# Kernel tuning notes

Measured on AMD Instinct MI355X. Metric: run time of the kernel, lower is better.

Reference implementation:

```python
import jax, jax.numpy as jnp
import numpy as np

N_COUNTS = 6  # pyramid levels (original + 5 sum-pools)


def _sum_pool2(x):
    # 2x2x2 sum pooling (AvgPool3d with divisor_override=1)
    B, C, D, H, W = x.shape
    return x.reshape(B, C, D // 2, 2, H // 2, 2, W // 2, 2).sum(axis=(3, 5, 7))


def _forward(image, bounds):
    n = N_COUNTS
    q = jnp.log(2.0 ** jnp.arange(n, dtype=jnp.float32))  # (S,)
    qs = q.sum()
    q2s = (q * q).sum()
    qs2 = qs * qs
    kf = bounds.astype(jnp.float32)  # (K,)
    # prefactor a: 1 for k==1 (entropy branch), else 1/(k-1); inf at k==1 masked by where
    a = jnp.where(bounds == 1, 1.0, 1.0 / jnp.where(bounds == 1, jnp.inf, kf - 1.0))

    # normalizer b = sum of nonzero entries of finest map == total sum
    b = image.sum(axis=(2, 3, 4))  # (B, C)

    maps = [image]
    for _ in range(n - 1):
        maps.append(_sum_pool2(maps[-1]))

    ps = []
    for m in maps:
        x = m.reshape(m.shape[0], m.shape[1], -1)  # (B, C, V)
        mask = x != 0
        xn = x / b[:, :, None]
        safe = jnp.where(mask, xn, 1.0)  # 1.0 placeholder at zeros, masked out below
        # generic branch (k != 1): p = log(sum over nonzero of (x/b)**k)
        pw = safe[:, :, :, None] ** kf  # (B, C, V, K)
        s = jnp.sum(jnp.where(mask[..., None], pw, 0.0), axis=2)  # (B, C, K)
        p_gen = jnp.log(s)
        # k == 1 branch: p = sum over nonzero of xn * log(xn)
        p_one = jnp.sum(jnp.where(mask, xn * jnp.log(safe), 0.0), axis=2)  # (B, C)
        ps.append(jnp.where(bounds == 1, p_one[:, :, None], p_gen))

    p_all = jnp.stack(ps, axis=-1)  # (B, C, K, S)
    # least-squares slope of p vs q; a00 = min(S, ql) = n
    num = n * jnp.einsum('bcks,s->bck', p_all, q) - p_all.sum(axis=-1) * qs
    den = n * q2s - qs2
    return a * num / den  # (B, C, K)


def setup_inputs() -> dict:
    key = jax.random.key(0)
    k1, _ = jax.random.split(key)
    image = jax.random.uniform(k1, (2, 3, 128, 128, 128), dtype=jnp.float32)
    bounds = jnp.arange(8, dtype=jnp.int32) - 2  # [-2..5]
    return {"image": image, "bounds": bounds}


def reference(image, bounds):
    return _forward(image, bounds)
```

## Files before the change

### kernel.cpp

```cpp
#include <hip/hip_runtime.h>

#define CHVOL (128*128*128)

__device__ __forceinline__ void accum9(float* a, float x) {
    bool nz = (x != 0.0f);
    float u = nz ? __builtin_amdgcn_rcpf(x) : 0.0f;
    float l = nz ? __logf(x) : 0.0f;
    float x2 = x * x;
    float x4 = x2 * x2;
    a[0] = fmaf(u, u, a[0]);
    a[1] += u;
    a[2] += nz ? 1.0f : 0.0f;
    a[3] += x;
    a[4] += x2;
    a[5] = fmaf(x2, x, a[5]);
    a[6] += x4;
    a[7] = fmaf(x4, x, a[7]);
    a[8] = fmaf(x, l, a[8]);
}

template<int NS>
__device__ __forceinline__ void wave_reduce(float* acc) {
    #pragma unroll
    for (int s = 0; s < NS; ++s) {
        float v = acc[s];
        v += __shfl_down(v, 32, 64);
        v += __shfl_down(v, 16, 64);
        v += __shfl_down(v, 8, 64);
        v += __shfl_down(v, 4, 64);
        v += __shfl_down(v, 2, 64);
        v += __shfl_down(v, 1, 64);
        acc[s] = v;
    }
}

template<int NS>
__device__ __forceinline__ void block_reduce(float* acc, float* red, int t) {
    #pragma unroll
    for (int s = 0; s < NS; ++s) {
        float v = acc[s];
        v += __shfl_down(v, 32, 64);
        v += __shfl_down(v, 16, 64);
        v += __shfl_down(v, 8, 64);
        v += __shfl_down(v, 4, 64);
        v += __shfl_down(v, 2, 64);
        v += __shfl_down(v, 1, 64);
        if ((t & 63) == 0) red[(t >> 6) * NS + s] = v;
    }
    __syncthreads();
}

__global__ __launch_bounds__(256) void k_main(const float* __restrict__ img,
                                              float* __restrict__ part,
                                              float* __restrict__ l3map) {
    __shared__ float zm[256];
    __shared__ float red[36 * 4];

    const int t  = threadIdx.x;
    const int l  = t & 63, w = t >> 6;
    const int r  = blockIdx.x;
    const int ch = blockIdx.y;
    const int ry = r & 15, rz = r >> 4;
    const float* base = img + (size_t)ch * CHVOL + rz * (8 * 16384) + ry * (8 * 128);

    float acc[36];
    #pragma unroll
    for (int j = 0; j < 36; ++j) acc[j] = 0.0f;

    const int x5 = l & 31;
    const int y  = ((l >> 5) & 1) | (w << 1);
    const float* tbase = base + y * 128 + x5 * 4;

    float4 v[8];
    #pragma unroll
    for (int i = 0; i < 8; ++i) v[i] = *(const float4*)(tbase + i * 16384);

    float d0 = 0.0f, d1 = 0.0f;
    float ca = 0.0f, cb = 0.0f;
    #pragma unroll
    for (int i = 0; i < 8; ++i) {
        accum9(acc, v[i].x); accum9(acc, v[i].y); accum9(acc, v[i].z); accum9(acc, v[i].w);
        float a = v[i].x + v[i].y, b = v[i].z + v[i].w;
        a += __shfl_xor(a, 32, 64);
        b += __shfl_xor(b, 32, 64);
        if ((i & 1) == 0) { ca = a; cb = b; }
        else {
            float A = ca + a, B = cb + b;
            accum9(acc + 9, A); accum9(acc + 9, B);
            if (i < 4) d0 += A + B; else d1 += A + B;
        }
    }
    #pragma unroll
    for (int j = 9; j < 18; ++j) acc[j] *= 0.5f;

    if ((l >> 5) == 0) {
        zm[w * 64 + x5]      = d0;
        zm[w * 64 + 32 + x5] = d1;
    }
    __syncthreads();

    if (t < 128) {
        int x = t & 31, zpp = (t >> 5) & 1, ypp = t >> 6;
        float s = zm[(2 * ypp) * 64 + zpp * 32 + x] + zm[(2 * ypp + 1) * 64 + zpp * 32 + x];
        accum9(acc + 18, s);
    }
    if (t < 16) {
        float s = 0.0f;
        #pragma unroll
        for (int q = 0; q < 8; ++q)
            s += zm[q * 32 + 2 * t] + zm[q * 32 + 2 * t + 1];
        accum9(acc + 27, s);
        l3map[(size_t)ch * 4096 + rz * 256 + ry * 16 + t] = s;
    }

    block_reduce<36>(acc, red, t);
    if (t < 36)
        part[((size_t)ch * 36 + t) * 256 + r] =
            red[t] + red[36 + t] + red[72 + t] + red[108 + t];
}

__global__ __launch_bounds__(512) void k_fin(const float* __restrict__ part,
                                             const float* __restrict__ l3map,
                                             const int* __restrict__ bounds,
                                             float* __restrict__ out) {
    __shared__ float M4[512];
    __shared__ float redA[36 * 4];
    __shared__ float redB[9 * 4];
    __shared__ float sst[54];

    const int t  = threadIdx.x;
    const int ch = blockIdx.x;

    if (t < 256) {
        float acc[36];
        #pragma unroll
        for (int j = 0; j < 36; ++j)
            acc[j] = part[((size_t)ch * 36 + j) * 256 + t];
        wave_reduce<36>(acc);
        if ((t & 63) == 0) {
            #pragma unroll
            for (int s = 0; s < 36; ++s) redA[(t >> 6) * 36 + s] = acc[s];
        }
    } else {
        const float2* L3 = (const float2*)(l3map + (size_t)ch * 4096);
        const int th = t - 256;
        float a9[9];
        #pragma unroll
        for (int j = 0; j < 9; ++j) a9[j] = 0.0f;
        #pragma unroll
        for (int i = 0; i < 2; ++i) {
            int c = th + i * 256;
            int x = c & 7, y = (c >> 3) & 7, z = c >> 6;
            const float2* p = L3 + z * 256 + y * 16 + x;
            float2 b0 = p[0], b1 = p[8], b2 = p[128], b3 = p[136];
            float s = (b0.x + b0.y) + (b1.x + b1.y) + (b2.x + b2.y) + (b3.x + b3.y);
            M4[c] = s;
            accum9(a9, s);
        }
        wave_reduce<9>(a9);
        if ((t & 63) == 0) {
            #pragma unroll
            for (int s = 0; s < 9; ++s) redB[((t >> 6) - 4) * 9 + s] = a9[s];
        }
    }
    __syncthreads();

    if (t < 36) sst[t] = redA[t] + redA[36 + t] + redA[72 + t] + redA[108 + t];
    if (t >= 36 && t < 45) {
        int s = t - 36;
        sst[36 + s] = redB[s] + redB[9 + s] + redB[18 + s] + redB[27 + s];
    }
    if (t < 64) {
        float c9[9];
        #pragma unroll
        for (int j = 0; j < 9; ++j) c9[j] = 0.0f;
        int x = t & 3, y = (t >> 2) & 3, z = t >> 4;
        const float2* p = (const float2*)M4 + z * 64 + y * 8 + x;
        float2 b0 = p[0], b1 = p[4], b2 = p[32], b3 = p[36];
        float s = (b0.x + b0.y) + (b1.x + b1.y) + (b2.x + b2.y) + (b3.x + b3.y);
        accum9(c9, s);
        wave_reduce<9>(c9);
        if (t == 0) {
            #pragma unroll
            for (int j = 0; j < 9; ++j) sst[45 + j] = c9[j];
        }
    }
    __syncthreads();

    if (t < 8) {
        int k = bounds[t];
        const double LN2 = 0.6931471805599453094;
        double b  = (double)sst[3];
        double lb = log(b);
        double num = 0.0;
        #pragma unroll
        for (int s = 0; s < 6; ++s) {
            const float* st = sst + s * 9;
            double p;
            if (k == 1) p = ((double)st[8] - lb * (double)st[3]) / b;
            else        p = log((double)st[k + 2]) - (double)k * lb;
            num += (6.0 * s - 15.0) * LN2 * p;
        }
        double den = 105.0 * LN2 * LN2;
        double aa  = (k == 1) ? 1.0 : 1.0 / (double)(k - 1);
        out[ch * 8 + t] = (float)(aa * num / den);
    }
}

extern "C" void kernel_launch(void* const* d_in, const int* in_sizes, int n_in,
                              void* d_out, int out_size, void* d_ws, size_t ws_size,
                              hipStream_t stream) {
    const float* img    = (const float*)d_in[0];
    const int*   bounds = (const int*)d_in[1];
    float*       out    = (float*)d_out;
    float*       ws     = (float*)d_ws;

    float* part  = ws;
    float* l3map = ws + 55296;

    k_main<<<dim3(256, 6), 256, 0, stream>>>(img, part, l3map);
    k_fin<<<6, 512, 0, stream>>>(part, l3map, bounds, out);
}
```

Baseline: 110.9 us.

## Remap threads so each owns a 2x2 y-z column, dropping level-1 shuffles

Each thread now loads 4 z-slices by 2 y-rows of a float4 column instead of 8 z-slices of one row. This lets it form complete 2x2x2 level-1 sums in registers, with no cross-lane shuffle exchange. The halving scale and the conditional even/odd pairing go away, and every thread writes one level-2 partial into shared memory. The trade-off is a less contiguous per-warp load pattern (two rows per z-slice rather than one), which could change coalescing.

```diff
diff --git a/kernel.cpp b/kernel.cpp
--- a/kernel.cpp
+++ b/kernel.cpp
@@ -57,46 +57,43 @@
     __shared__ float red[36 * 4];
 
     const int t  = threadIdx.x;
-    const int l  = t & 63, w = t >> 6;
     const int r  = blockIdx.x;
     const int ch = blockIdx.y;
     const int ry = r & 15, rz = r >> 4;
-    const float* base = img + (size_t)ch * CHVOL + rz * (8 * 16384) + ry * (8 * 128);
+
+    const int x5 = t & 31;
+    const int yp = (t >> 5) & 3;
+    const int zq = t >> 7;
+
+    const float* tb = img + (size_t)ch * CHVOL + rz * (8 * 16384) + ry * (8 * 128)
+                    + (zq * 4) * 16384 + (yp * 2) * 128 + x5 * 4;
 
     float acc[36];
     #pragma unroll
     for (int j = 0; j < 36; ++j) acc[j] = 0.0f;
 
-    const int x5 = l & 31;
-    const int y  = ((l >> 5) & 1) | (w << 1);
-    const float* tbase = base + y * 128 + x5 * 4;
-
     float4 v[8];
     #pragma unroll
-    for (int i = 0; i < 8; ++i) v[i] = *(const float4*)(tbase + i * 16384);
-
-    float d0 = 0.0f, d1 = 0.0f;
-    float ca = 0.0f, cb = 0.0f;
+    for (int dz = 0; dz < 4; ++dz)
+        #pragma unroll
+        for (int dy = 0; dy < 2; ++dy)
+            v[dz * 2 + dy] = *(const float4*)(tb + dz * 16384 + dy * 128);
+
     #pragma unroll
     for (int i = 0; i < 8; ++i) {
         accum9(acc, v[i].x); accum9(acc, v[i].y); accum9(acc, v[i].z); accum9(acc, v[i].w);
-        float a = v[i].x + v[i].y, b = v[i].z + v[i].w;
-        a += __shfl_xor(a, 32, 64);
-        b += __shfl_xor(b, 32, 64);
-        if ((i & 1) == 0) { ca = a; cb = b; }
-        else {
-            float A = ca + a, B = cb + b;
-            accum9(acc + 9, A); accum9(acc + 9, B);
-            if (i < 4) d0 += A + B; else d1 += A + B;
-        }
-    }
-    #pragma unroll
-    for (int j = 9; j < 18; ++j) acc[j] *= 0.5f;
-
-    if ((l >> 5) == 0) {
-        zm[w * 64 + x5]      = d0;
-        zm[w * 64 + 32 + x5] = d1;
-    }
+    }
+
+    float ax[8], bx[8];
+    #pragma unroll
+    for (int i = 0; i < 8; ++i) { ax[i] = v[i].x + v[i].y; bx[i] = v[i].z + v[i].w; }
+    float A0 = (ax[0] + ax[1]) + (ax[2] + ax[3]);
+    float B0 = (bx[0] + bx[1]) + (bx[2] + bx[3]);
+    float A1 = (ax[4] + ax[5]) + (ax[6] + ax[7]);
+    float B1 = (bx[4] + bx[5]) + (bx[6] + bx[7]);
+    accum9(acc + 9, A0); accum9(acc + 9, B0); accum9(acc + 9, A1); accum9(acc + 9, B1);
+
+    zm[yp * 64 + zq * 32 + x5] = (A0 + B0) + (A1 + B1);
     __syncthreads();
 
     if (t < 128) {
```

Result: slower. 115.3 us (+4.0%).
